# Kernel optimization log

Hardware: AMD Instinct MI355X
Metric: run time of the kernel (lower is better)

Reference implementation:

```python
import jax, jax.numpy as jnp
import numpy as np

N_ROWS = 100000   # sparse matrix rows (nodes)
N_COLS = 8192     # input feature dim
UNITS = 128
NNZ = 2000000     # ~20 nonzeros per row


def setup_inputs() -> dict:
    key = jax.random.key(0)
    k1, k2, k3, k4, k5 = jax.random.split(key, 5)
    vals = jax.random.normal(k1, (NNZ,), dtype=jnp.float32)
    rows = jax.random.randint(k2, (NNZ,), 0, N_ROWS, dtype=jnp.int32)
    cols = jax.random.randint(k3, (NNZ,), 0, N_COLS, dtype=jnp.int32)
    # GlorotUniform-style scale for W, matching the TF initializer statistics
    limit = jnp.sqrt(6.0 / (N_COLS + UNITS)).astype(jnp.float32)
    W = jax.random.uniform(k4, (N_COLS, UNITS), dtype=jnp.float32, minval=-limit, maxval=limit)
    b = jax.random.uniform(k5, (UNITS,), dtype=jnp.float32, minval=-limit, maxval=limit)
    return {"vals": vals, "rows": rows, "cols": cols, "W": W, "b": b, "num_rows": N_ROWS}


def reference(vals, rows, cols, W, b, num_rows):
    # sparse (COO) [num_rows, F] @ dense W [F, units]:
    # gather the W row for each nonzero, scale by the nonzero value,
    # then scatter-add into the output row -> segment_sum over `rows`.
    gathered = W[cols] * vals[:, None]            # [nnz, units]
    out = jax.ops.segment_sum(gathered, rows, num_segments=num_rows)  # [num_rows, units]
    return out + b                                 # bias add (use_bias=True)
```

## Files before the change

kernel.cpp:

```cpp
#include <hip/hip_runtime.h>
#include <hip/hip_fp16.h>


#define UNITS 128
#define SCAN_BLK 1024
#define BROW 98
#define CBROW 784
#define NCC 128
#define CCAP 17664
#define CH3 2048
#define STCAP 2816
#define SPILL_CAP 8192


__global__ __launch_bounds__(512, 8) void partition_kernel(
        const float* __restrict__ vals, const int* __restrict__ rows,
        const int* __restrict__ cols, const float* __restrict__ W,
        __half2* __restrict__ Wh, int* __restrict__ ccur,
        float2* __restrict__ sortedA, float2* __restrict__ spill,
        int nnz, int nbcc, int wn2) {
    __shared__ unsigned short invs[CH3];
    __shared__ int hist[NCC];
    __shared__ int gdelta[NCC];

    const int t = threadIdx.x;
    const int lane = t & 63;
    const int w = t >> 6;
    const int bb = blockIdx.x;

    {
        const float2* W2 = (const float2*)W;
        int stride = gridDim.x * 512;
        for (int i = bb * 512 + t; i < wn2; i += stride)
            Wh[i] = __float22half2_rn(W2[i]);
    }

    const int chunk0 = bb * CH3;
    int n = nnz - chunk0;
    if (n > CH3) n = CH3;

    if (t < NCC) hist[t] = 0;
    __syncthreads();

    int bk[4];
#pragma unroll
    for (int j = 0; j < 4; ++j) {
        int r = j * 512 + t;
        int bkt = -1;
        if (r < n) {
            bkt = rows[chunk0 + r] / CBROW;
            atomicAdd(&hist[bkt], 1);
        }
        bk[j] = bkt;
    }
    __syncthreads();

    if (w == 0) {
        int a0 = hist[2 * lane], a1 = hist[2 * lane + 1];
        int ps = a0 + a1;
        int inc = ps;
#pragma unroll
        for (int o = 1; o < 64; o <<= 1) {
            int u = __shfl_up(inc, o);
            if (lane >= o) inc += u;
        }
        int excl = inc - ps;
        int s0 = 2 * lane, s1 = 2 * lane + 1;
        int g0 = (s0 < nbcc && a0 > 0) ? atomicAdd(&ccur[s0 * 16], a0) : 0;
        int g1 = (s1 < nbcc && a1 > 0) ? atomicAdd(&ccur[s1 * 16], a1) : 0;
        gdelta[s0] = s0 * CCAP + g0 - excl;
        gdelta[s1] = s1 * CCAP + g1 - (excl + a0);
        hist[s0] = excl;
        hist[s1] = excl + a0;
    }
    __syncthreads();

#pragma unroll
    for (int j = 0; j < 4; ++j) {
        int bkt = bk[j];
        if (bkt >= 0) {
            int pos = atomicAdd(&hist[bkt], 1);
            invs[pos] = (unsigned short)(j * 512 + t);
        }
    }
    __syncthreads();

    int* spill_cnt = &ccur[NCC * 16];
    for (int s = t; s < n; s += 512) {
        int r = invs[s];
        int i = chunk0 + r;
        int row = rows[i];
        float v = vals[i];
        int col = cols[i];
        int bkt = row / CBROW;
        int rlo = row - bkt * CBROW;
        int dest = gdelta[bkt] + s;
        if (dest < (bkt + 1) * CCAP) {
            sortedA[dest] = make_float2(v, __int_as_float(col | (rlo << 13)));
        } else {
            int sp = atomicAdd(spill_cnt, 1);
            if (sp < SPILL_CAP)
                spill[sp] = make_float2(v, __int_as_float(col | (row << 13)));
        }
    }
}


__global__ __launch_bounds__(512, 8) void fused_sort_compute_kernel(
        const float2* __restrict__ A, const int* __restrict__ ccur,
        const __half2* __restrict__ Wh, const float* __restrict__ b,
        float* __restrict__ out, const float2* __restrict__ spill, int NR) {
    __shared__ float2 st[STCAP + 8];
    __shared__ int cnt_s[128];
    __shared__ int rs[129];
    __shared__ int spill_n;
    const int t = threadIdx.x;
    const int lane = t & 63;
    const int w = t >> 6;

    const int nwg = gridDim.x;
    const int orig = blockIdx.x;
    const int q = nwg >> 3, r8 = nwg & 7, xcd = orig & 7, idx = orig >> 3;
    const int f = (xcd < r8 ? xcd * (q + 1) : r8 * (q + 1) + (xcd - r8) * q) + idx;

    const int c = f >> 3, sb = f & 7;
    const int r0 = f * BROW;
    const int rlo0 = sb * BROW;
    const size_t base = (size_t)c * CCAP;
    int segn = ccur[c * 16];
    if (segn > CCAP) segn = CCAP;

    const float2 bias = ((const float2*)b)[lane];

    if (t < 128) cnt_s[t] = 0;
    if (t == 0) {
        int sn = ccur[NCC * 16];
        spill_n = (sn > SPILL_CAP) ? SPILL_CAP : sn;
    }
    __syncthreads();

    const int* Ai = (const int*)(A + base);
    for (int k = t; k < segn; k += 512) {
        unsigned rl = (unsigned)(Ai[2 * k + 1] >> 13) - rlo0;
        if (rl < BROW) atomicAdd(&cnt_s[rl], 1);
    }
    __syncthreads();

    if (t < 128) rs[t] = (cnt_s[t] + 3) & ~3;
    __syncthreads();
    for (int off = 1; off < 128; off <<= 1) {
        int v = (t < 128 && t >= off) ? rs[t - off] : 0;
        __syncthreads();
        if (t < 128) rs[t] += v;
        __syncthreads();
    }
    int rc = (t < 128) ? ((cnt_s[t] + 3) & ~3) : 0;
    int excl = (t < 128) ? rs[t] - rc : 0;
    __syncthreads();
    if (t < 128) {
        rs[t] = (excl < STCAP) ? excl : STCAP;
        cnt_s[t] = excl;
    }
    if (t == 127) {
        int tot = excl + rc;
        rs[128] = (tot < STCAP) ? tot : STCAP;
    }
    for (int i = t; i < STCAP + 8; i += 512) st[i] = make_float2(0.f, __int_as_float(0));
    __syncthreads();

    for (int k = t; k < segn; k += 512) {
        float2 e = A[base + k];
        int pk = __float_as_int(e.y);
        unsigned rl = (unsigned)(pk >> 13) - rlo0;
        if (rl < BROW) {
            int p = atomicAdd(&cnt_s[rl], 1);
            if (p < STCAP) st[p] = make_float2(e.x, __int_as_float(pk & 8191));
        }
    }
    __syncthreads();

    const int sn = spill_n;
    for (int r = w; r < BROW; r += 8) {
        int grow = r0 + r;
        if (grow >= NR) break;
        int s4 = rs[r], e4 = rs[r + 1];
        float ax0 = 0.f, ay0 = 0.f, ax1 = 0.f, ay1 = 0.f;
        for (int k = s4; k < e4; k += 4) {
            float2 p0 = st[k];
            float2 p1 = st[k + 1];
            float2 p2 = st[k + 2];
            float2 p3 = st[k + 3];
            int c0 = __float_as_int(p0.y) & 8191;
            int c1 = __float_as_int(p1.y) & 8191;
            int c2 = __float_as_int(p2.y) & 8191;
            int c3 = __float_as_int(p3.y) & 8191;
            float2 w0 = __half22float2(Wh[c0 * 64 + lane]);
            float2 w1 = __half22float2(Wh[c1 * 64 + lane]);
            float2 w2 = __half22float2(Wh[c2 * 64 + lane]);
            float2 w3 = __half22float2(Wh[c3 * 64 + lane]);
            ax0 += p0.x * w0.x; ay0 += p0.x * w0.y;
            ax1 += p1.x * w1.x; ay1 += p1.x * w1.y;
            ax0 += p2.x * w2.x; ay0 += p2.x * w2.y;
            ax1 += p3.x * w3.x; ay1 += p3.x * w3.y;
        }
        for (int s2 = 0; s2 < sn; ++s2) {
            float2 es = spill[s2];
            int pk = __float_as_int(es.y);
            if ((pk >> 13) == grow) {
                float2 wv = __half22float2(Wh[(pk & 8191) * 64 + lane]);
                ax0 += es.x * wv.x; ay0 += es.x * wv.y;
            }
        }
        ((float2*)out)[(size_t)grow * 64 + lane] =
            make_float2(ax0 + ax1 + bias.x, ay0 + ay1 + bias.y);
    }
}


__global__ void hist_kernel(const int* __restrict__ rows, int* __restrict__ counts, int nnz) {
    int i = blockIdx.x * blockDim.x + threadIdx.x;
    if (i < nnz) atomicAdd(&counts[rows[i]], 1);
}

__global__ void scan1_kernel(const int* __restrict__ counts, int* __restrict__ tmp,
                             int* __restrict__ bsums, int NR, int NS) {
    __shared__ int s[SCAN_BLK];
    int t = threadIdx.x;
    int i = blockIdx.x * SCAN_BLK + t;
    int x = (i < NR) ? counts[i] : 0;
    s[t] = x;
    __syncthreads();
    for (int off = 1; off < SCAN_BLK; off <<= 1) {
        int v = (t >= off) ? s[t - off] : 0;
        __syncthreads();
        s[t] += v;
        __syncthreads();
    }
    if (i < NS) tmp[i] = s[t] - x;
    if (t == SCAN_BLK - 1) bsums[blockIdx.x] = s[SCAN_BLK - 1];
}

__global__ void scan2_kernel(int* __restrict__ bsums, int nb) {
    if (threadIdx.x == 0 && blockIdx.x == 0) {
        int run = 0;
        for (int i = 0; i < nb; ++i) { int c = bsums[i]; bsums[i] = run; run += c; }
    }
}

__global__ void scan3_kernel(const int* __restrict__ tmp, const int* __restrict__ bsums,
                             int* __restrict__ row_start, int* __restrict__ cursor,
                             int NR, int NS) {
    int i = blockIdx.x * blockDim.x + threadIdx.x;
    if (i < NS) {
        int v = tmp[i] + bsums[i >> 10];
        row_start[i] = v;
        if (i < NR) cursor[i] = v;
    }
}

__global__ void scatter_sort_kernel(const float* __restrict__ vals, const int* __restrict__ rows,
                                    const int* __restrict__ cols, int* __restrict__ cursor,
                                    float2* __restrict__ sorted, int nnz) {
    int i = blockIdx.x * blockDim.x + threadIdx.x;
    if (i < nnz) {
        int r = rows[i];
        int p = atomicAdd(&cursor[r], 1);
        sorted[p] = make_float2(vals[i], __int_as_float(cols[i]));
    }
}

__global__ void compute_kernel(const float2* __restrict__ sorted, const int* __restrict__ row_start,
                               const float* __restrict__ W, const float* __restrict__ b,
                               float* __restrict__ out, int NR) {
    int lane = threadIdx.x & 63;
    int wv = threadIdx.x >> 6;
    int row = blockIdx.x * 4 + wv;
    if (row >= NR) return;
    int start = row_start[row];
    int end   = row_start[row + 1];
    const float2* W2 = (const float2*)W;
    float accx0 = 0.f, accy0 = 0.f, accx1 = 0.f, accy1 = 0.f;
    for (int base = start; base < end; base += 64) {
        int m = end - base;
        if (m > 64) m = 64;
        float2 p = make_float2(0.f, __int_as_float(0));
        if (lane < m) p = sorted[base + lane];
        int vi = __float_as_int(p.x);
        int ci = __float_as_int(p.y);
        int rounds = (m + 3) & ~3;
        for (int j = 0; j < rounds; j += 4) {
            float v0 = __int_as_float(__builtin_amdgcn_readlane(vi, j));
            int   c0 = __builtin_amdgcn_readlane(ci, j);
            float v1 = __int_as_float(__builtin_amdgcn_readlane(vi, j + 1));
            int   c1 = __builtin_amdgcn_readlane(ci, j + 1);
            float v2 = __int_as_float(__builtin_amdgcn_readlane(vi, j + 2));
            int   c2 = __builtin_amdgcn_readlane(ci, j + 2);
            float v3 = __int_as_float(__builtin_amdgcn_readlane(vi, j + 3));
            int   c3 = __builtin_amdgcn_readlane(ci, j + 3);
            float2 w0 = W2[c0 * 64 + lane];
            float2 w1 = W2[c1 * 64 + lane];
            float2 w2 = W2[c2 * 64 + lane];
            float2 w3 = W2[c3 * 64 + lane];
            accx0 += v0 * w0.x; accy0 += v0 * w0.y;
            accx1 += v1 * w1.x; accy1 += v1 * w1.y;
            accx0 += v2 * w2.x; accy0 += v2 * w2.y;
            accx1 += v3 * w3.x; accy1 += v3 * w3.y;
        }
    }
    float2 bb = ((const float2*)b)[lane];
    ((float2*)out)[(size_t)row * 64 + lane] =
        make_float2(accx0 + accx1 + bb.x, accy0 + accy1 + bb.y);
}


__global__ void init_bias_kernel(float* __restrict__ out, const float* __restrict__ b, int total4) {
    const float4* b4 = (const float4*)b;
    float4* out4 = (float4*)out;
    int stride = gridDim.x * blockDim.x;
    for (int j = blockIdx.x * blockDim.x + threadIdx.x; j < total4; j += stride)
        out4[j] = b4[j & 31];
}

__global__ void scatter_atomic_kernel(const float* __restrict__ vals, const int* __restrict__ rows,
                                      const int* __restrict__ cols, const float* __restrict__ W,
                                      float* __restrict__ out, int nnz) {
    long long idx = (long long)blockIdx.x * blockDim.x + threadIdx.x;
    int i = (int)(idx >> 5);
    int c = (int)(idx & 31);
    if (i >= nnz) return;
    int row = rows[i], col = cols[i];
    float v = vals[i];
    float4 w = ((const float4*)W)[col * 32 + c];
    float* o = out + (size_t)row * UNITS + (c << 2);
    atomicAdd(o + 0, v * w.x);
    atomicAdd(o + 1, v * w.y);
    atomicAdd(o + 2, v * w.z);
    atomicAdd(o + 3, v * w.w);
}

extern "C" void kernel_launch(void* const* d_in, const int* in_sizes, int n_in,
                              void* d_out, int out_size, void* d_ws, size_t ws_size,
                              hipStream_t stream) {
    const float* vals = (const float*)d_in[0];
    const int*   rows = (const int*)d_in[1];
    const int*   cols = (const int*)d_in[2];
    const float* W    = (const float*)d_in[3];
    const float* b    = (const float*)d_in[4];
    float* out = (float*)d_out;

    const int nnz = in_sizes[0];
    const int NW  = in_sizes[3];
    const int NR  = out_size / UNITS;
    const int NS  = NR + 1;
    const int NB  = (NS + SCAN_BLK - 1) / SCAN_BLK;
    const int nbf  = (NR + BROW - 1) / BROW;
    const int nbcc = (NR + CBROW - 1) / CBROW;

    auto align = [](size_t x) { return (x + 255) & ~(size_t)255; };

    size_t off_ccur    = 0;
    size_t off_wh      = align(off_ccur + (size_t)(NCC * 16 + 1) * 4);
    size_t off_sortedA = align(off_wh + (size_t)NW * 2);
    size_t off_spill   = align(off_sortedA + (size_t)NCC * CCAP * 8);
    size_t needed_full = off_spill + (size_t)SPILL_CAP * 8;

    size_t t2_counts   = 0;
    size_t t2_tmp      = align(t2_counts + (size_t)NR * 4);
    size_t t2_bsums    = align(t2_tmp    + (size_t)NS * 4);
    size_t t2_rowstart = align(t2_bsums  + (size_t)NB * 4);
    size_t t2_cursor   = align(t2_rowstart + (size_t)NS * 4);
    size_t t2_sorted   = align(t2_cursor + (size_t)NR * 4);
    size_t needed_r2   = t2_sorted + (size_t)nnz * 8;

    char* ws = (char*)d_ws;

    if (ws_size >= needed_full && nbcc >= 1 && nbcc <= NCC && NR >= 1) {
        int*     ccur    = (int*)(ws + off_ccur);
        __half2* Wh      = (__half2*)(ws + off_wh);
        float2*  sortedA = (float2*)(ws + off_sortedA);
        float2*  spill   = (float2*)(ws + off_spill);

        hipMemsetAsync(ccur, 0, (size_t)(NCC * 16 + 1) * 4, stream);
        {
            int grid = (nnz + CH3 - 1) / CH3;
            partition_kernel<<<grid, 512, 0, stream>>>(vals, rows, cols, W, Wh,
                                                       ccur, sortedA, spill,
                                                       nnz, nbcc, NW / 2);
        }
        fused_sort_compute_kernel<<<nbf, 512, 0, stream>>>(sortedA, ccur, Wh, b,
                                                           out, spill, NR);
    } else if (ws_size >= needed_r2) {
        int*    counts    = (int*)(ws + t2_counts);
        int*    tmp       = (int*)(ws + t2_tmp);
        int*    bsums     = (int*)(ws + t2_bsums);
        int*    row_start = (int*)(ws + t2_rowstart);
        int*    cursor    = (int*)(ws + t2_cursor);
        float2* sorted    = (float2*)(ws + t2_sorted);

        hipMemsetAsync(counts, 0, (size_t)NR * 4, stream);
        {
            int block = 256, grid = (nnz + block - 1) / block;
            hist_kernel<<<grid, block, 0, stream>>>(rows, counts, nnz);
        }
        scan1_kernel<<<NB, SCAN_BLK, 0, stream>>>(counts, tmp, bsums, NR, NS);
        scan2_kernel<<<1, 64, 0, stream>>>(bsums, NB);
        {
            int block = 256, grid = (NS + block - 1) / block;
            scan3_kernel<<<grid, block, 0, stream>>>(tmp, bsums, row_start, cursor, NR, NS);
        }
        {
            int block = 256, grid = (nnz + block - 1) / block;
            scatter_sort_kernel<<<grid, block, 0, stream>>>(vals, rows, cols, cursor, sorted, nnz);
        }
        {
            int grid = (NR + 3) / 4;
            compute_kernel<<<grid, 256, 0, stream>>>(sorted, row_start, W, b, out, NR);
        }
    } else {
        int total4 = out_size / 4;
        int block = 256;
        int grid = (total4 + block - 1) / block;
        init_bias_kernel<<<grid, block, 0, stream>>>(out, b, total4);
        long long total_threads = (long long)nnz * 32;
        long long g2 = (total_threads + block - 1) / block;
        scatter_atomic_kernel<<<(int)g2, block, 0, stream>>>(vals, rows, cols, W, out, nnz);
    }
}
```

Before: 182.8 us.

## Use fixed per-row slots with overflow and stage partition entries in LDS

The compute kernel no longer counts entries per row and prefix-scans before bucketing. It places each entry directly into a fixed 40-slot region per row and sends extras to a small shared overflow list. The partition kernel stages packed entries in shared memory during the first pass instead of re-reading rows, vals and cols by index later. This removes a global read pass, a barrier-heavy scan and buffer zeroing. In exchange it uses more LDS, adds a linear overflow scan per row, and reads unmasked padding slots.

```diff
diff --git a/kernel.cpp b/kernel.cpp
--- a/kernel.cpp
+++ b/kernel.cpp
@@ -9,7 +9,8 @@
 #define NCC 128
 #define CCAP 17664
 #define CH3 2048
-#define STCAP 2816
+#define SLOTS 40
+#define OVF_CAP 256
 #define SPILL_CAP 8192
 
 
@@ -19,7 +20,8 @@
         __half2* __restrict__ Wh, int* __restrict__ ccur,
         float2* __restrict__ sortedA, float2* __restrict__ spill,
         int nnz, int nbcc, int wn2) {
-    __shared__ unsigned short invs[CH3];
+    __shared__ float2 sStage[CH3];
+    __shared__ unsigned short sBkt[CH3];
     __shared__ int hist[NCC];
     __shared__ int gdelta[NCC];
 
@@ -42,16 +44,16 @@
     if (t < NCC) hist[t] = 0;
     __syncthreads();
 
-    int bk[4];
+    int rbuf[4];
 #pragma unroll
     for (int j = 0; j < 4; ++j) {
         int r = j * 512 + t;
-        int bkt = -1;
+        int rv = -1;
         if (r < n) {
-            bkt = rows[chunk0 + r] / CBROW;
-            atomicAdd(&hist[bkt], 1);
-        }
-        bk[j] = bkt;
+            rv = rows[chunk0 + r];
+            atomicAdd(&hist[rv / CBROW], 1);
+        }
+        rbuf[j] = rv;
     }
     __syncthreads();
 
@@ -77,30 +79,34 @@
 
 #pragma unroll
     for (int j = 0; j < 4; ++j) {
-        int bkt = bk[j];
-        if (bkt >= 0) {
+        int rv = rbuf[j];
+        if (rv >= 0) {
+            int r = j * 512 + t;
+            int bkt = rv / CBROW;
+            int rlo = rv - bkt * CBROW;
             int pos = atomicAdd(&hist[bkt], 1);
-            invs[pos] = (unsigned short)(j * 512 + t);
+            float v = vals[chunk0 + r];
+            int col = cols[chunk0 + r];
+            sStage[pos] = make_float2(v, __int_as_float(col | (rlo << 13)));
+            sBkt[pos] = (unsigned short)bkt;
         }
     }
     __syncthreads();
 
     int* spill_cnt = &ccur[NCC * 16];
     for (int s = t; s < n; s += 512) {
-        int r = invs[s];
-        int i = chunk0 + r;
-        int row = rows[i];
-        float v = vals[i];
-        int col = cols[i];
-        int bkt = row / CBROW;
-        int rlo = row - bkt * CBROW;
+        float2 e = sStage[s];
+        int bkt = sBkt[s];
         int dest = gdelta[bkt] + s;
         if (dest < (bkt + 1) * CCAP) {
-            sortedA[dest] = make_float2(v, __int_as_float(col | (rlo << 13)));
+            sortedA[dest] = e;
         } else {
             int sp = atomicAdd(spill_cnt, 1);
-            if (sp < SPILL_CAP)
-                spill[sp] = make_float2(v, __int_as_float(col | (row << 13)));
+            if (sp < SPILL_CAP) {
+                int pk = __float_as_int(e.y);
+                int row = bkt * CBROW + (pk >> 13);
+                spill[sp] = make_float2(e.x, __int_as_float((pk & 8191) | (row << 13)));
+            }
         }
     }
 }
@@ -110,9 +116,10 @@
         const float2* __restrict__ A, const int* __restrict__ ccur,
         const __half2* __restrict__ Wh, const float* __restrict__ b,
         float* __restrict__ out, const float2* __restrict__ spill, int NR) {
-    __shared__ float2 st[STCAP + 8];
-    __shared__ int cnt_s[128];
-    __shared__ int rs[129];
+    __shared__ float2 st[BROW * SLOTS];
+    __shared__ float2 ovf[OVF_CAP];
+    __shared__ int cnt_s[BROW + 6];
+    __shared__ int ovf_n;
     __shared__ int spill_n;
     const int t = threadIdx.x;
     const int lane = t & 63;
@@ -132,40 +139,12 @@
 
     const float2 bias = ((const float2*)b)[lane];
 
-    if (t < 128) cnt_s[t] = 0;
+    if (t < BROW + 6) cnt_s[t] = 0;
     if (t == 0) {
+        ovf_n = 0;
         int sn = ccur[NCC * 16];
         spill_n = (sn > SPILL_CAP) ? SPILL_CAP : sn;
     }
-    __syncthreads();
-
-    const int* Ai = (const int*)(A + base);
-    for (int k = t; k < segn; k += 512) {
-        unsigned rl = (unsigned)(Ai[2 * k + 1] >> 13) - rlo0;
-        if (rl < BROW) atomicAdd(&cnt_s[rl], 1);
-    }
-    __syncthreads();
-
-    if (t < 128) rs[t] = (cnt_s[t] + 3) & ~3;
-    __syncthreads();
-    for (int off = 1; off < 128; off <<= 1) {
-        int v = (t < 128 && t >= off) ? rs[t - off] : 0;
-        __syncthreads();
-        if (t < 128) rs[t] += v;
-        __syncthreads();
-    }
-    int rc = (t < 128) ? ((cnt_s[t] + 3) & ~3) : 0;
-    int excl = (t < 128) ? rs[t] - rc : 0;
-    __syncthreads();
-    if (t < 128) {
-        rs[t] = (excl < STCAP) ? excl : STCAP;
-        cnt_s[t] = excl;
-    }
-    if (t == 127) {
-        int tot = excl + rc;
-        rs[128] = (tot < STCAP) ? tot : STCAP;
-    }
-    for (int i = t; i < STCAP + 8; i += 512) st[i] = make_float2(0.f, __int_as_float(0));
     __syncthreads();
 
     for (int k = t; k < segn; k += 512) {
@@ -174,34 +153,55 @@
         unsigned rl = (unsigned)(pk >> 13) - rlo0;
         if (rl < BROW) {
             int p = atomicAdd(&cnt_s[rl], 1);
-            if (p < STCAP) st[p] = make_float2(e.x, __int_as_float(pk & 8191));
-        }
-    }
-    __syncthreads();
-
+            if (p < SLOTS) {
+                st[rl * SLOTS + p] = make_float2(e.x, __int_as_float(pk & 8191));
+            } else {
+                int qn = atomicAdd(&ovf_n, 1);
+                if (qn < OVF_CAP)
+                    ovf[qn] = make_float2(e.x, __int_as_float((pk & 8191) | (rl << 13)));
+            }
+        }
+    }
+    __syncthreads();
+
+    const int on = (ovf_n > OVF_CAP) ? OVF_CAP : ovf_n;
     const int sn = spill_n;
     for (int r = w; r < BROW; r += 8) {
         int grow = r0 + r;
         if (grow >= NR) break;
-        int s4 = rs[r], e4 = rs[r + 1];
+        int cnt = cnt_s[r];
+        if (cnt > SLOTS) cnt = SLOTS;
+        const float2* strow = &st[r * SLOTS];
         float ax0 = 0.f, ay0 = 0.f, ax1 = 0.f, ay1 = 0.f;
-        for (int k = s4; k < e4; k += 4) {
-            float2 p0 = st[k];
-            float2 p1 = st[k + 1];
-            float2 p2 = st[k + 2];
-            float2 p3 = st[k + 3];
+        for (int k = 0; k < cnt; k += 4) {
+            float2 p0 = strow[k];
+            float2 p1 = strow[k + 1];
+            float2 p2 = strow[k + 2];
+            float2 p3 = strow[k + 3];
             int c0 = __float_as_int(p0.y) & 8191;
             int c1 = __float_as_int(p1.y) & 8191;
             int c2 = __float_as_int(p2.y) & 8191;
             int c3 = __float_as_int(p3.y) & 8191;
+            float v0 = p0.x;
+            float v1 = (k + 1 < cnt) ? p1.x : 0.f;
+            float v2 = (k + 2 < cnt) ? p2.x : 0.f;
+            float v3 = (k + 3 < cnt) ? p3.x : 0.f;
             float2 w0 = __half22float2(Wh[c0 * 64 + lane]);
             float2 w1 = __half22float2(Wh[c1 * 64 + lane]);
             float2 w2 = __half22float2(Wh[c2 * 64 + lane]);
             float2 w3 = __half22float2(Wh[c3 * 64 + lane]);
-            ax0 += p0.x * w0.x; ay0 += p0.x * w0.y;
-            ax1 += p1.x * w1.x; ay1 += p1.x * w1.y;
-            ax0 += p2.x * w2.x; ay0 += p2.x * w2.y;
-            ax1 += p3.x * w3.x; ay1 += p3.x * w3.y;
+            ax0 += v0 * w0.x; ay0 += v0 * w0.y;
+            ax1 += v1 * w1.x; ay1 += v1 * w1.y;
+            ax0 += v2 * w2.x; ay0 += v2 * w2.y;
+            ax1 += v3 * w3.x; ay1 += v3 * w3.y;
+        }
+        for (int q2 = 0; q2 < on; ++q2) {
+            float2 eo = ovf[q2];
+            int pk = __float_as_int(eo.y);
+            if ((pk >> 13) == r) {
+                float2 wv = __half22float2(Wh[(pk & 8191) * 64 + lane]);
+                ax0 += eo.x * wv.x; ay0 += eo.x * wv.y;
+            }
         }
         for (int s2 = 0; s2 < sn; ++s2) {
             float2 es = spill[s2];
```

Result: faster. 171.1 us (-6.4%).
